# Kernel tuning notes

Hardware: AMD Instinct MI355X
Metric: run time of the kernel (lower is better)

The kernel has to match this reference:

```python
import jax, jax.numpy as jnp
import numpy as np

T, D, E, K = 16384, 4096, 64, 2


def setup_inputs() -> dict:
    key = jax.random.key(0)
    k1, k2, k3 = jax.random.split(key, 3)
    x = jax.random.normal(k1, (T, D), dtype=jnp.float32)
    # torch nn.Linear default init scale ~ 1/sqrt(fan_in)
    gate_w = jax.random.normal(k2, (E, D), dtype=jnp.float32) * (1.0 / np.sqrt(D))
    gate_b = jax.random.normal(k3, (E,), dtype=jnp.float32) * (1.0 / np.sqrt(D))
    return {"x": x, "gate_w": gate_w, "gate_b": gate_b}


def reference(x, gate_w, gate_b):
    # gate linear: [T, D] @ [D, E] + [E] -> [T, E]
    router_logits = jnp.einsum("td,ed->te", x, gate_w) + gate_b
    # softmax over experts in float32 (matches F.softmax(..., dtype=torch.float))
    router_probs = jax.nn.softmax(router_logits.astype(jnp.float32), axis=-1)
    # top-k experts per token
    router_weights, select_expert_indices = jax.lax.top_k(router_probs, K)  # [T, K]
    # renormalize selected weights to sum to 1
    router_weights = router_weights / jnp.sum(router_weights, axis=-1, keepdims=True)
    router_weights = router_weights.astype(x.dtype)
    # one-hot mask [T, K, E] -> permute(2,1,0) -> [E, K, T]
    expert_mask = jax.nn.one_hot(select_expert_indices, E, dtype=jnp.int32)
    expert_mask = jnp.transpose(expert_mask, (2, 1, 0))
    return (router_logits, router_weights, select_expert_indices, expert_mask)
```

## Files before the change

kernel.cpp:

```cpp
#include <hip/hip_runtime.h>
#include <math.h>

#define T_TOK 16384
#define D_DIM 4096
#define E_EXP 64

#define OFF_W   (T_TOK * E_EXP)
#define OFF_I   (OFF_W + T_TOK * 2)
#define OFF_M   (OFF_I + T_TOK * 2)

#define NCHUNK    64
#define CH_HALVES 4096

typedef _Float16 half8 __attribute__((ext_vector_type(8)));
typedef float    f32x4 __attribute__((ext_vector_type(4)));

__global__ __launch_bounds__(256) void prep_w(const float* __restrict__ w,
                                              _Float16* __restrict__ ws_hi,
                                              _Float16* __restrict__ ws_lo) {
  const int g   = blockIdx.x * 256 + threadIdx.x;
  const int exp = g >> 8;
  const int kb  = (g & 255) * 16;
  const float* src = w + (size_t)exp * D_DIM + kb;
  float vals[16];
#pragma unroll
  for (int i = 0; i < 4; i++) {
    const float4 f = *(const float4*)(src + i * 4);
    vals[i * 4 + 0] = f.x; vals[i * 4 + 1] = f.y;
    vals[i * 4 + 2] = f.z; vals[i * 4 + 3] = f.w;
  }
  const int n_tile = exp >> 4, nn = exp & 15;
#pragma unroll
  for (int part = 0; part < 2; part++) {
    const int k0 = kb + part * 8;
    const int c = k0 >> 6, rem = k0 & 63;
    const int s = rem >> 5, q = (rem >> 3) & 3;
    const size_t off = (size_t)c * CH_HALVES + (n_tile * 2 + s) * 512 + (nn + 16 * q) * 8;
    half8 hv, lv;
#pragma unroll
    for (int j = 0; j < 8; j++) {
      const float xf = vals[part * 8 + j];
      const _Float16 h = (_Float16)xf;
      hv[j] = h;
      lv[j] = (_Float16)((xf - (float)h) * 2048.0f);
    }
    *(half8*)(ws_hi + off) = hv;
    *(half8*)(ws_lo + off) = lv;
  }
}

__global__ __launch_bounds__(256, 1) void moe_mfma(
    const float* __restrict__ x, const _Float16* __restrict__ ws_hi,
    const _Float16* __restrict__ ws_lo, const float* __restrict__ bias,
    float* __restrict__ out) {
  __shared__ __align__(16) _Float16 smem[2][4][CH_HALVES];

  const int tid  = threadIdx.x;
  const int wave = tid >> 6;
  const int lane = tid & 63;
  const int tok0 = blockIdx.x * 64;
  const int stok = tid >> 2;
  const int so4  = tid & 3;

  f32x4 accm[4], accc[4];
#pragma unroll
  for (int t = 0; t < 4; t++) {
    accm[t] = (f32x4){0.f, 0.f, 0.f, 0.f};
    accc[t] = (f32x4){0.f, 0.f, 0.f, 0.f};
  }

  float4 xr[2][4];
  uint4  br[2][4];

  auto loadx = [&](int c, float4* xv) {
    const float* p = x + (size_t)(tok0 + stok) * D_DIM + c * 64 + so4 * 8;
    xv[0] = ((const float4*)p)[0];
    xv[1] = ((const float4*)p)[1];
    xv[2] = ((const float4*)(p + 32))[0];
    xv[3] = ((const float4*)(p + 32))[1];
  };
  auto loadB = [&](int c, uint4* bv) {
    const uint4* ph = (const uint4*)(ws_hi + (size_t)c * CH_HALVES) + tid * 2;
    bv[0] = ph[0]; bv[1] = ph[1];
    const uint4* pl = (const uint4*)(ws_lo + (size_t)c * CH_HALVES) + tid * 2;
    bv[2] = pl[0]; bv[3] = pl[1];
  };
  auto stage = [&](int buf, const float4* xv, const uint4* bv) {
    const int g = stok >> 4, m = stok & 15;
#pragma unroll
    for (int p = 0; p < 2; p++) {
      const int o = so4 + 4 * p;
      const int s = o >> 2, q = o & 3;
      const int off = (g * 2 + s) * 512 + (m + 16 * q) * 8;
      const float4 f0 = xv[2 * p], f1 = xv[2 * p + 1];
      const float vv[8] = {f0.x, f0.y, f0.z, f0.w, f1.x, f1.y, f1.z, f1.w};
      half8 hv, lv;
#pragma unroll
      for (int j = 0; j < 8; j++) {
        const _Float16 h = (_Float16)vv[j];
        hv[j] = h;
        lv[j] = (_Float16)((vv[j] - (float)h) * 2048.0f);
      }
      *(half8*)(&smem[buf][0][off]) = hv;
      *(half8*)(&smem[buf][1][off]) = lv;
    }
    *(uint4*)(&smem[buf][2][tid * 16])     = bv[0];
    *(uint4*)(&smem[buf][2][tid * 16 + 8]) = bv[1];
    *(uint4*)(&smem[buf][3][tid * 16])     = bv[2];
    *(uint4*)(&smem[buf][3][tid * 16 + 8]) = bv[3];
  };
  auto compute = [&](int buf) {
#pragma unroll
    for (int s = 0; s < 2; s++) {
      const half8 ah = *(const half8*)(&smem[buf][0][(wave * 2 + s) * 512 + lane * 8]);
      const half8 al = *(const half8*)(&smem[buf][1][(wave * 2 + s) * 512 + lane * 8]);
#pragma unroll
      for (int t = 0; t < 4; t++) {
        const half8 bh = *(const half8*)(&smem[buf][2][(t * 2 + s) * 512 + lane * 8]);
        const half8 bl = *(const half8*)(&smem[buf][3][(t * 2 + s) * 512 + lane * 8]);
        accm[t] = __builtin_amdgcn_mfma_f32_16x16x32_f16(ah, bh, accm[t], 0, 0, 0);
        accc[t] = __builtin_amdgcn_mfma_f32_16x16x32_f16(ah, bl, accc[t], 0, 0, 0);
        accc[t] = __builtin_amdgcn_mfma_f32_16x16x32_f16(al, bh, accc[t], 0, 0, 0);
      }
    }
  };

  loadx(0, xr[0]); loadB(0, br[0]);
  stage(0, xr[0], br[0]);
  loadx(1, xr[1]); loadB(1, br[1]);
  __syncthreads();
#pragma unroll 1
  for (int c = 0; c < NCHUNK; c += 2) {
    if (c + 2 < NCHUNK) { loadx(c + 2, xr[0]); loadB(c + 2, br[0]); }
    compute(0);
    stage(1, xr[1], br[1]);
    __syncthreads();
    if (c + 3 < NCHUNK) { loadx(c + 3, xr[1]); loadB(c + 3, br[1]); }
    compute(1);
    if (c + 2 < NCHUNK) stage(0, xr[0], br[0]);
    __syncthreads();
  }

  const int cc = lane & 15, q = lane >> 4;
  float fin[4][4];
#pragma unroll
  for (int t = 0; t < 4; t++) {
    const float bb = bias[t * 16 + cc];
#pragma unroll
    for (int r = 0; r < 4; r++)
      fin[t][r] = accm[t][r] + accc[t][r] * 4.8828125e-4f + bb;
  }
#pragma unroll
  for (int r = 0; r < 4; r++) {
    const int trow = tok0 + wave * 16 + q * 4 + r;
#pragma unroll
    for (int t = 0; t < 4; t++)
      out[(size_t)trow * E_EXP + t * 16 + cc] = fin[t][r];
  }

#pragma unroll
  for (int r = 0; r < 4; r++) {
    float v1 = fin[0][r]; int i1 = cc;
    float v2 = -3.4e38f;  int i2 = 0;
#pragma unroll
    for (int t = 1; t < 4; t++) {
      const float vc = fin[t][r]; const int ic = t * 16 + cc;
      if (vc > v1)      { v2 = v1; i2 = i1; v1 = vc; i1 = ic; }
      else if (vc > v2) { v2 = vc; i2 = ic; }
    }
#pragma unroll
    for (int mk = 1; mk <= 8; mk <<= 1) {
      const float ov1 = __shfl_xor(v1, mk); const int oi1 = __shfl_xor(i1, mk);
      const float ov2 = __shfl_xor(v2, mk); const int oi2 = __shfl_xor(i2, mk);
      if ((ov1 > v1) || (ov1 == v1 && oi1 < i1)) {
        const bool s2 = (v1 > ov2) || (v1 == ov2 && i1 < oi2);
        v2 = s2 ? v1 : ov2; i2 = s2 ? i1 : oi2;
        v1 = ov1; i1 = oi1;
      } else {
        const bool s2 = (ov1 > v2) || (ov1 == v2 && oi1 < i2);
        v2 = s2 ? ov1 : v2; i2 = s2 ? oi1 : i2;
      }
    }
    if (cc == 0) {
      const int trow = tok0 + wave * 16 + q * 4 + r;
      const float d  = expf(v2 - v1);
      const float w1 = 1.f / (1.f + d);
      out[OFF_W + trow * 2 + 0] = w1;
      out[OFF_W + trow * 2 + 1] = d * w1;
      out[OFF_I + trow * 2 + 0] = (float)i1;
      out[OFF_I + trow * 2 + 1] = (float)i2;
      out[OFF_M + (size_t)(i1 * 2 + 0) * T_TOK + trow] = 1.0f;
      out[OFF_M + (size_t)(i2 * 2 + 1) * T_TOK + trow] = 1.0f;
    }
  }
}

extern "C" void kernel_launch(void* const* d_in, const int* in_sizes, int n_in,
                              void* d_out, int out_size, void* d_ws, size_t ws_size,
                              hipStream_t stream) {
  const float* x    = (const float*)d_in[0];
  const float* w    = (const float*)d_in[1];
  const float* bias = (const float*)d_in[2];
  float* out = (float*)d_out;
  _Float16* ws_hi = (_Float16*)d_ws;
  _Float16* ws_lo = ws_hi + (size_t)NCHUNK * CH_HALVES;

  hipMemsetAsync(out + OFF_M, 0, (size_t)E_EXP * 2 * T_TOK * sizeof(float), stream);
  prep_w<<<E_EXP * D_DIM / (256 * 16), 256, 0, stream>>>(w, ws_hi, ws_lo);
  moe_mfma<<<T_TOK / 64, 256, 0, stream>>>(x, ws_hi, ws_lo, bias, out);
}
```

Measured before the change: 437.1 us.

## Drop LDS staging; load A and B fragments directly into registers per wave

The shared-memory double buffer and block-wide barriers are removed. Each lane now loads its own x fragment straight from global memory in MFMA operand layout and splits it to fp16 hi/lo in registers. Each wave loads its own B fragments from the pre-swizzled weight buffer, with a 4-deep A prefetch and a 2-deep B prefetch. The launch-bounds occupancy hint of 1 is also dropped, which allows more blocks per CU. In exchange, every wave reloads the full B weights from L2 instead of sharing one LDS copy, and x reads become 32-byte strided per lane.

```diff
diff --git a/kernel.cpp b/kernel.cpp
--- a/kernel.cpp
+++ b/kernel.cpp
@@ -49,18 +49,17 @@
   }
 }
 
-__global__ __launch_bounds__(256, 1) void moe_mfma(
+__global__ __launch_bounds__(256) void moe_mfma(
     const float* __restrict__ x, const _Float16* __restrict__ ws_hi,
     const _Float16* __restrict__ ws_lo, const float* __restrict__ bias,
     float* __restrict__ out) {
-  __shared__ __align__(16) _Float16 smem[2][4][CH_HALVES];
-
   const int tid  = threadIdx.x;
   const int wave = tid >> 6;
   const int lane = tid & 63;
-  const int tok0 = blockIdx.x * 64;
-  const int stok = tid >> 2;
-  const int so4  = tid & 3;
+  const int m    = lane & 15;
+  const int q    = lane >> 4;
+  const int trowbase = blockIdx.x * 64 + wave * 16;
+  const float* xrow = x + (size_t)(trowbase + m) * D_DIM + q * 8;
 
   f32x4 accm[4], accc[4];
 #pragma unroll
@@ -69,79 +68,58 @@
     accc[t] = (f32x4){0.f, 0.f, 0.f, 0.f};
   }
 
-  float4 xr[2][4];
-  uint4  br[2][4];
+  float4 abuf[4][2];
+  uint4  bh[2][4], bl[2][4];
 
-  auto loadx = [&](int c, float4* xv) {
-    const float* p = x + (size_t)(tok0 + stok) * D_DIM + c * 64 + so4 * 8;
-    xv[0] = ((const float4*)p)[0];
-    xv[1] = ((const float4*)p)[1];
-    xv[2] = ((const float4*)(p + 32))[0];
-    xv[3] = ((const float4*)(p + 32))[1];
+  auto aload = [&](int ks, int slot) {
+    const float* p = xrow + (ks >> 1) * 64 + (ks & 1) * 32;
+    abuf[slot][0] = *(const float4*)p;
+    abuf[slot][1] = *(const float4*)(p + 4);
   };
-  auto loadB = [&](int c, uint4* bv) {
-    const uint4* ph = (const uint4*)(ws_hi + (size_t)c * CH_HALVES) + tid * 2;
-    bv[0] = ph[0]; bv[1] = ph[1];
-    const uint4* pl = (const uint4*)(ws_lo + (size_t)c * CH_HALVES) + tid * 2;
-    bv[2] = pl[0]; bv[3] = pl[1];
+  auto bload = [&](int ks, int pb) {
+    const size_t base = (size_t)(ks >> 1) * CH_HALVES + (ks & 1) * 512 + lane * 8;
+    const _Float16* ph = ws_hi + base;
+    const _Float16* pl = ws_lo + base;
+#pragma unroll
+    for (int t = 0; t < 4; t++) {
+      bh[pb][t] = *(const uint4*)(ph + t * 1024);
+      bl[pb][t] = *(const uint4*)(pl + t * 1024);
+    }
   };
-  auto stage = [&](int buf, const float4* xv, const uint4* bv) {
-    const int g = stok >> 4, m = stok & 15;
+  auto comp = [&](int slot, int pb) {
+    const float4 f0 = abuf[slot][0], f1 = abuf[slot][1];
+    const float vv[8] = {f0.x, f0.y, f0.z, f0.w, f1.x, f1.y, f1.z, f1.w};
+    half8 ah, al;
 #pragma unroll
-    for (int p = 0; p < 2; p++) {
-      const int o = so4 + 4 * p;
-      const int s = o >> 2, q = o & 3;
-      const int off = (g * 2 + s) * 512 + (m + 16 * q) * 8;
-      const float4 f0 = xv[2 * p], f1 = xv[2 * p + 1];
-      const float vv[8] = {f0.x, f0.y, f0.z, f0.w, f1.x, f1.y, f1.z, f1.w};
-      half8 hv, lv;
+    for (int j = 0; j < 8; j++) {
+      const _Float16 h = (_Float16)vv[j];
+      ah[j] = h;
+      al[j] = (_Float16)((vv[j] - (float)h) * 2048.0f);
+    }
 #pragma unroll
-      for (int j = 0; j < 8; j++) {
-        const _Float16 h = (_Float16)vv[j];
-        hv[j] = h;
-        lv[j] = (_Float16)((vv[j] - (float)h) * 2048.0f);
-      }
-      *(half8*)(&smem[buf][0][off]) = hv;
-      *(half8*)(&smem[buf][1][off]) = lv;
-    }
-    *(uint4*)(&smem[buf][2][tid * 16])     = bv[0];
-    *(uint4*)(&smem[buf][2][tid * 16 + 8]) = bv[1];
-    *(uint4*)(&smem[buf][3][tid * 16])     = bv[2];
-    *(uint4*)(&smem[buf][3][tid * 16 + 8]) = bv[3];
-  };
-  auto compute = [&](int buf) {
-#pragma unroll
-    for (int s = 0; s < 2; s++) {
-      const half8 ah = *(const half8*)(&smem[buf][0][(wave * 2 + s) * 512 + lane * 8]);
-      const half8 al = *(const half8*)(&smem[buf][1][(wave * 2 + s) * 512 + lane * 8]);
-#pragma unroll
-      for (int t = 0; t < 4; t++) {
-        const half8 bh = *(const half8*)(&smem[buf][2][(t * 2 + s) * 512 + lane * 8]);
-        const half8 bl = *(const half8*)(&smem[buf][3][(t * 2 + s) * 512 + lane * 8]);
-        accm[t] = __builtin_amdgcn_mfma_f32_16x16x32_f16(ah, bh, accm[t], 0, 0, 0);
-        accc[t] = __builtin_amdgcn_mfma_f32_16x16x32_f16(ah, bl, accc[t], 0, 0, 0);
-        accc[t] = __builtin_amdgcn_mfma_f32_16x16x32_f16(al, bh, accc[t], 0, 0, 0);
-      }
+    for (int t = 0; t < 4; t++) {
+      const half8 bhv = *(const half8*)&bh[pb][t];
+      const half8 blv = *(const half8*)&bl[pb][t];
+      accm[t] = __builtin_amdgcn_mfma_f32_16x16x32_f16(ah, bhv, accm[t], 0, 0, 0);
+      accc[t] = __builtin_amdgcn_mfma_f32_16x16x32_f16(ah, blv, accc[t], 0, 0, 0);
+      accc[t] = __builtin_amdgcn_mfma_f32_16x16x32_f16(al, bhv, accc[t], 0, 0, 0);
     }
   };
 
-  loadx(0, xr[0]); loadB(0, br[0]);
-  stage(0, xr[0], br[0]);
-  loadx(1, xr[1]); loadB(1, br[1]);
-  __syncthreads();
+  aload(0, 0); aload(1, 1); aload(2, 2); aload(3, 3);
+  bload(0, 0); bload(1, 1);
+
 #pragma unroll 1
-  for (int c = 0; c < NCHUNK; c += 2) {
-    if (c + 2 < NCHUNK) { loadx(c + 2, xr[0]); loadB(c + 2, br[0]); }
-    compute(0);
-    stage(1, xr[1], br[1]);
-    __syncthreads();
-    if (c + 3 < NCHUNK) { loadx(c + 3, xr[1]); loadB(c + 3, br[1]); }
-    compute(1);
-    if (c + 2 < NCHUNK) stage(0, xr[0], br[0]);
-    __syncthreads();
+  for (int ks = 0; ks < 128; ks += 2) {
+    comp(ks & 3, 0);
+    if (ks + 4 < 128) aload(ks + 4, (ks + 4) & 3);
+    if (ks + 2 < 128) bload(ks + 2, 0);
+    comp((ks + 1) & 3, 1);
+    if (ks + 5 < 128) aload(ks + 5, (ks + 5) & 3);
+    if (ks + 3 < 128) bload(ks + 3, 1);
   }
 
-  const int cc = lane & 15, q = lane >> 4;
+  const int cc = lane & 15;
   float fin[4][4];
 #pragma unroll
   for (int t = 0; t < 4; t++) {
@@ -152,7 +130,7 @@
   }
 #pragma unroll
   for (int r = 0; r < 4; r++) {
-    const int trow = tok0 + wave * 16 + q * 4 + r;
+    const int trow = trowbase + q * 4 + r;
 #pragma unroll
     for (int t = 0; t < 4; t++)
       out[(size_t)trow * E_EXP + t * 16 + cc] = fin[t][r];
@@ -182,7 +160,7 @@
       }
     }
     if (cc == 0) {
-      const int trow = tok0 + wave * 16 + q * 4 + r;
+      const int trow = trowbase + q * 4 + r;
       const float d  = expf(v2 - v1);
       const float w1 = 1.f / (1.f + d);
       out[OFF_W + trow * 2 + 0] = w1;
```

Measured after the change: 490.3 us. +12.2%, slower.
